# Optimization experiments

Hardware: AMD Instinct MI355X
Metric: run time of the kernel (lower is better)

## Reference

```python
import jax, jax.numpy as jnp
import numpy as np

N = 128          # system size (8*8*2), hard-coded in SpectrumLoss
M_LANCZOS = 10   # Lanczos(m=10)
KAPPA = 0.276


def dd_opt(x, U1, kappa):
    # Wilson-style 2D hopping operator (stand-in for the external DDOpt).
    # x: (B,8,8,2) fields, U1: (B,8,8,2) real gauge links (2 directions).
    u0 = U1[..., 0:1]
    u1 = U1[..., 1:2]
    hop = (u0 * jnp.roll(x, -1, axis=1)
           + u1 * jnp.roll(x, -1, axis=2)
           + jnp.roll(u0 * x, 1, axis=1)
           + jnp.roll(u1 * x, 1, axis=2))
    return x - kappa * hop


def build_lower_tri(net_out):
    # Row-major packing of a lower-triangular NxN matrix (torch.tril_indices order).
    B = net_out.shape[0]
    r, c = jnp.tril_indices(N)
    L = jnp.zeros((B, N, N), net_out.dtype)
    return L.at[:, r, c].set(net_out)


def matvect(L, U1, x):
    # x: (B, N). Preconditioned operator: L (L^T (D x)).
    B = x.shape[0]
    y = dd_opt(x.reshape(B, 8, 8, 2), U1, KAPPA).reshape(B, N)
    y = jnp.einsum('bij,bi->bj', L, y)  # upper_tri_mat: M^H v (real -> M^T v)
    y = jnp.einsum('bij,bj->bi', L, y)  # lower_tri_matvect: L v
    return y


def lanczos(Av, v0):
    # Standard batched Lanczos producing symmetric tridiagonal T (B, M, M).
    B = v0.shape[0]

    def step(carry, _):
        v_prev, v_cur, beta = carry
        w = Av(v_cur)
        alpha = jnp.sum(w * v_cur, axis=1)
        w = w - alpha[:, None] * v_cur - beta[:, None] * v_prev
        beta_new = jnp.linalg.norm(w, axis=1)
        v_next = w / (beta_new[:, None] + 1e-30)
        return (v_cur, v_next, beta_new), (alpha, beta_new)

    init = (jnp.zeros_like(v0), v0, jnp.zeros((B,), v0.dtype))
    _, (alphas, betas) = jax.lax.scan(step, init, None, length=M_LANCZOS)
    alphas = alphas.T  # (B, M)
    betas = betas.T    # (B, M); last beta unused
    T = jnp.zeros((B, M_LANCZOS, M_LANCZOS), v0.dtype)
    i = jnp.arange(M_LANCZOS)
    T = T.at[:, i, i].set(alphas)
    j = jnp.arange(M_LANCZOS - 1)
    T = T.at[:, j, j + 1].set(betas[:, :-1])
    T = T.at[:, j + 1, j].set(betas[:, :-1])
    return T


def setup_inputs() -> dict:
    key = jax.random.key(0)
    k1, k2, k3 = jax.random.split(key, 3)
    B = 2048
    net_out = jax.random.normal(k1, (B, N * (N + 1) // 2), dtype=jnp.float32)
    U1 = jax.random.uniform(k2, (B, 8, 8, 2), dtype=jnp.float32)
    v = jax.random.normal(k3, (B, N), dtype=jnp.float32)
    return {"net_out": net_out, "U1": U1, "v": v}


def reference(net_out, U1, v):
    vn = v / jnp.linalg.norm(v, axis=1, keepdims=True)
    L = build_lower_tri(net_out)
    T = lanczos(lambda x: matvect(L, U1, x), vn)
    eig = jnp.abs(jnp.linalg.eigvalsh(T))  # symmetric tridiagonal -> real eigvals
    max_e = jnp.max(eig, axis=1)
    min_e = jnp.min(eig, axis=1)
    return jnp.mean(max_e ** 2) - jnp.mean(min_e ** 2)
```

## Files before the change

### kernel.cpp

```cpp
#include <hip/hip_runtime.h>
#include <hip/hip_bf16.h>
#include <math.h>

#define NN 128
#define TRI 8256
#define BATCH 2048
#define M_L 10
#define KAPPA 0.276f
#define LDL 136

using half8  = __attribute__((ext_vector_type(8))) _Float16;
using half2v = __attribute__((ext_vector_type(2))) _Float16;
using f32x4  = __attribute__((ext_vector_type(4))) float;

static __device__ inline float dot2h(unsigned m, unsigned y, float c) {
#if __has_builtin(__builtin_amdgcn_fdot2)
    return __builtin_amdgcn_fdot2(__builtin_bit_cast(half2v, m),
                                  __builtin_bit_cast(half2v, y), c, false);
#else
    half2v a = __builtin_bit_cast(half2v, m), b = __builtin_bit_cast(half2v, y);
    return c + (float)a.x * (float)b.x + (float)a.y * (float)b.y;
#endif
}

__global__ __launch_bounds__(256, 4) void lanczos_kernel(
    const float* __restrict__ net_out,
    const float* __restrict__ U1,
    const float* __restrict__ v_in,
    float* __restrict__ ab_out)
{
    __shared__ __align__(16) _Float16 Lsq[128 * LDL];
    __shared__ float u0s[64], u1s[64];
    __shared__ __align__(16) float xv[NN];
    __shared__ __align__(16) _Float16 yh[NN];
    __shared__ float red[6];

    const int b = blockIdx.x;
    const int t = threadIdx.x;
    const int lane = t & 63;
    const int w = t >> 6;

    {
        unsigned long long* z = (unsigned long long*)Lsq;
        #pragma unroll
        for (int k = t; k < 128 * LDL * 2 / 8; k += 256) z[k] = 0ULL;
    }
    if (t < 64) {
        const float2* uu = (const float2*)(U1 + (size_t)b * 128);
        float2 p = uu[t];
        u0s[t] = p.x; u1s[t] = p.y;
    }
    float vt = 0.0f;
    if (t < 128) vt = v_in[(size_t)b * NN + t];
    __syncthreads();

    {
        const float4* src4 = (const float4*)(net_out + (size_t)b * TRI);
        for (int q = t; q < TRI / 4; q += 256) {
            float4 f = src4[q];
            int e = 4 * q;
            int r = (int)((sqrtf(8.0f * (float)e + 1.0f) - 1.0f) * 0.5f);
            while ((r + 1) * (r + 2) / 2 <= e) r++;
            while (r * (r + 1) / 2 > e) r--;
            int c = e - r * (r + 1) / 2;
            Lsq[r * LDL + c] = (_Float16)f.x;
            c++; if (c > r) { r++; c = 0; }
            Lsq[r * LDL + c] = (_Float16)f.y;
            c++; if (c > r) { r++; c = 0; }
            Lsq[r * LDL + c] = (_Float16)f.z;
            c++; if (c > r) { r++; c = 0; }
            Lsq[r * LDL + c] = (_Float16)f.w;
        }
    }
    {
        float s = vt * vt;
        #pragma unroll
        for (int o = 32; o > 0; o >>= 1) s += __shfl_down(s, o, 64);
        if (lane == 0 && t < 128) red[w] = s;
    }
    __syncthreads();

    float xcur = 0.0f;
    if (t < 128) {
        float nrm = sqrtf(red[0] + red[1]);
        xcur = vt / nrm;
        xv[t] = xcur;
    }

    {
        const int m = lane & 15;
        const int g = lane >> 4;
        f32x4 acc[2][8];
        #pragma unroll
        for (int bi = 0; bi < 2; bi++)
            #pragma unroll
            for (int j = 0; j < 8; j++) acc[bi][j] = (f32x4){0.f, 0.f, 0.f, 0.f};
        const int band0 = w, band1 = w + 4;
        #pragma unroll
        for (int kc = 0; kc < 4; kc++) {
            const int col = kc * 32 + g * 8;
            half8 a0 = *(const half8*)&Lsq[(16 * band0 + m) * LDL + col];
            half8 a1 = *(const half8*)&Lsq[(16 * band1 + m) * LDL + col];
            #pragma unroll
            for (int j = 0; j < 8; j++) {
                half8 bfr = *(const half8*)&Lsq[(16 * j + m) * LDL + col];
                acc[0][j] = __builtin_amdgcn_mfma_f32_16x16x32_f16(a0, bfr, acc[0][j], 0, 0, 0);
                acc[1][j] = __builtin_amdgcn_mfma_f32_16x16x32_f16(a1, bfr, acc[1][j], 0, 0, 0);
            }
        }
        __syncthreads();

        #pragma unroll
        for (int bi = 0; bi < 2; bi++) {
            const int band = (bi == 0) ? band0 : band1;
            #pragma unroll
            for (int j = 0; j < 8; j++) {
                f32x4 a = acc[bi][j];
                half2v p01 = {(_Float16)a[0], (_Float16)a[1]};
                half2v p23 = {(_Float16)a[2], (_Float16)a[3]};
                uint2 pk;
                pk.x = __builtin_bit_cast(unsigned, p01);
                pk.y = __builtin_bit_cast(unsigned, p23);
                *(uint2*)&Lsq[(16 * j + m) * LDL + 16 * band + 4 * g] = pk;
            }
        }
    }

    const int si = t >> 4, sj = (t >> 1) & 7, ss = t & 1;
    const int ip = (si + 1) & 7, im = (si + 7) & 7;
    const int jp = (sj + 1) & 7, jm = (sj + 7) & 7;
    const int idx_ip = (ip << 4) | (sj << 1) | ss;
    const int idx_jp = (si << 4) | (jp << 1) | ss;
    const int idx_im = (im << 4) | (sj << 1) | ss;
    const int idx_jm = (si << 4) | (jm << 1) | ss;

    float pvf = 0.0f, beta = 0.0f;
    __syncthreads();

    for (int m_it = 0; m_it < M_L; m_it++) {
        if (t < 128) {
            float hop = u0s[si * 8 + sj] * xv[idx_ip]
                      + u1s[si * 8 + sj] * xv[idx_jp]
                      + u0s[im * 8 + sj] * xv[idx_im]
                      + u1s[si * 8 + jm] * xv[idx_jm];
            yh[t] = (_Float16)(xcur - KAPPA * hop);
        }
        __syncthreads();

        float z = 0.0f;
        if (t < 128) {
            const uint4* M4 = (const uint4*)&Lsq[t * LDL];
            const uint4* Y4 = (const uint4*)yh;
            float acc = 0.f;
            #pragma unroll
            for (int c = 0; c < 16; c++) {
                uint4 mv = M4[c];
                uint4 yv4 = Y4[c];
                acc = dot2h(mv.x, yv4.x, acc);
                acc = dot2h(mv.y, yv4.y, acc);
                acc = dot2h(mv.z, yv4.z, acc);
                acc = dot2h(mv.w, yv4.w, acc);
            }
            z = acc;
            float s1 = z * xcur;
            float s2 = z * z;
            float s3 = z * pvf;
            #pragma unroll
            for (int o = 32; o > 0; o >>= 1) {
                s1 += __shfl_down(s1, o, 64);
                s2 += __shfl_down(s2, o, 64);
                s3 += __shfl_down(s3, o, 64);
            }
            if (lane == 0) { red[w] = s1; red[2 + w] = s2; red[4 + w] = s3; }
        }
        __syncthreads();

        if (t < 128) {
            float alpha = red[0] + red[1];
            float z2    = red[2] + red[3];
            float zp    = red[4] + red[5];
            float b2 = z2 - alpha * alpha - beta * (2.0f * zp - beta);
            float beta_new = sqrtf(fmaxf(b2, 0.0f));
            float wv = z - alpha * xcur - beta * pvf;
            float xn = wv / (beta_new + 1e-30f);
            pvf = xcur;
            xcur = xn;
            xv[t] = xn;
            beta = beta_new;
            if (t == 0) {
                ab_out[(size_t)b * 20 + m_it]      = alpha;
                ab_out[(size_t)b * 20 + 10 + m_it] = beta_new;
            }
        }
        __syncthreads();
    }
}

__device__ inline int sturm_count10(const double* a, const double* off2, double x) {
    double pm = 1.0;
    double p  = a[0] - x;
    int c = (p < 0.0);
    #pragma unroll
    for (int i = 1; i < M_L; i++) {
        double pn = (a[i] - x) * p - off2[i - 1] * pm;
        c += ((pn < 0.0) != (p < 0.0));
        if (fabs(pn) > 1e150) { pn *= 1e-150; p *= 1e-150; }
        pm = p; p = pn;
    }
    return c;
}

__device__ inline double msect_smallest(const double* a, const double* off2,
                                        double lo, double hi, int K, int lane) {
    for (int round = 0; round < 4; round++) {
        double wdt = (hi - lo) * (1.0 / 65.0);
        double x = lo + wdt * (double)(lane + 1);
        int cnt = sturm_count10(a, off2, x);
        unsigned long long mask = __ballot(cnt >= K);
        if (mask == 0ULL) {
            lo = lo + wdt * 64.0;
        } else {
            int p = __ffsll(mask) - 1;
            hi = lo + wdt * (double)(p + 1);
            if (p > 0) lo = lo + wdt * (double)p;
        }
    }
    return 0.5 * (lo + hi);
}

__device__ inline double msect_window(const double* a, const double* off2,
                                      double maxabs, int lane) {
    double lo = 0.0, hi = maxabs;
    for (int round = 0; round < 4; round++) {
        double wdt = (hi - lo) * (1.0 / 65.0);
        double s = lo + wdt * (double)(lane + 1);
        int inwin = sturm_count10(a, off2, s) - sturm_count10(a, off2, -s);
        unsigned long long mask = __ballot(inwin >= 1);
        if (mask == 0ULL) {
            lo = lo + wdt * 64.0;
        } else {
            int p = __ffsll(mask) - 1;
            hi = lo + wdt * (double)(p + 1);
            if (p > 0) lo = lo + wdt * (double)p;
        }
    }
    return 0.5 * (lo + hi);
}

__global__ __launch_bounds__(256) void eig_kernel(
    const float* __restrict__ ab, float* __restrict__ contrib)
{
    const int lane = threadIdx.x & 63;
    const int b = blockIdx.x * 4 + (threadIdx.x >> 6);
    if (b >= BATCH) return;
    const float* p = ab + (size_t)b * 20;
    double a[M_L], off2[M_L - 1], offa[M_L - 1];
    #pragma unroll
    for (int i = 0; i < M_L; i++) a[i] = (double)p[i];
    #pragma unroll
    for (int i = 0; i < M_L - 1; i++) {
        double bb = (double)p[10 + i];
        offa[i] = fabs(bb);
        off2[i] = bb * bb;
    }
    double lo = 1e300, hi = -1e300;
    #pragma unroll
    for (int i = 0; i < M_L; i++) {
        double r = 0.0;
        if (i > 0) r += offa[i - 1];
        if (i < M_L - 1) r += offa[i];
        lo = fmin(lo, a[i] - r);
        hi = fmax(hi, a[i] + r);
    }
    double lmax = msect_smallest(a, off2, lo, hi, M_L, lane);
    double lmin = msect_smallest(a, off2, lo, hi, 1,   lane);
    double maxabs = fmax(fabs(lmax), fabs(lmin));
    double minabs = msect_window(a, off2, maxabs, lane);
    if (lane == 0) contrib[b] = (float)(maxabs * maxabs - minabs * minabs);
}

__global__ __launch_bounds__(1024) void reduce_kernel(
    const float* __restrict__ contrib, float* __restrict__ out)
{
    __shared__ float red[16];
    int t = threadIdx.x;
    float s = contrib[t] + contrib[t + 1024];
    #pragma unroll
    for (int o = 32; o > 0; o >>= 1) s += __shfl_down(s, o, 64);
    if ((t & 63) == 0) red[t >> 6] = s;
    __syncthreads();
    if (t < 64) {
        float r = (t < 16) ? red[t] : 0.0f;
        #pragma unroll
        for (int o = 8; o > 0; o >>= 1) r += __shfl_down(r, o, 64);
        if (t == 0) out[0] = r / (float)BATCH;
    }
}

extern "C" void kernel_launch(void* const* d_in, const int* in_sizes, int n_in,
                              void* d_out, int out_size, void* d_ws, size_t ws_size,
                              hipStream_t stream) {
    const float* net_out = (const float*)d_in[0];
    const float* U1      = (const float*)d_in[1];
    const float* v       = (const float*)d_in[2];
    float* ab      = (float*)d_ws;
    float* contrib = ab + (size_t)BATCH * 20;

    lanczos_kernel<<<BATCH, 256, 0, stream>>>(net_out, U1, v, ab);
    eig_kernel<<<BATCH / 4, 256, 0, stream>>>(ab, contrib);
    reduce_kernel<<<1, 1024, 0, stream>>>(contrib, (float*)d_out);
}
```

Baseline: 140.1 us.

## Process four batch items per block with one wave per Lanczos iteration

Each block now handles four batch elements in turn. All four waves still cooperate to build L and the MFMA product L·L^T for each element in shared memory. The wave that owns an element then loads its two matrix rows into registers and runs the ten Lanczos iterations entirely within the wave, using shuffles for the stencil and the reductions. This removes the block-wide barriers and idle threads of the old per-iteration loop, but it costs 128 registers of matrix per thread, serialises the four matrix builds inside a block, and drops occupancy.

```diff
diff --git a/kernel.cpp b/kernel.cpp
--- a/kernel.cpp
+++ b/kernel.cpp
@@ -23,176 +23,170 @@
 #endif
 }
 
-__global__ __launch_bounds__(256, 4) void lanczos_kernel(
+__global__ __launch_bounds__(256, 2) void lanczos_kernel(
     const float* __restrict__ net_out,
     const float* __restrict__ U1,
     const float* __restrict__ v_in,
     float* __restrict__ ab_out)
 {
     __shared__ __align__(16) _Float16 Lsq[128 * LDL];
-    __shared__ float u0s[64], u1s[64];
-    __shared__ __align__(16) float xv[NN];
-    __shared__ __align__(16) _Float16 yh[NN];
-    __shared__ float red[6];
-
-    const int b = blockIdx.x;
+    __shared__ __align__(16) unsigned yscr[4][64];
+
     const int t = threadIdx.x;
     const int lane = t & 63;
     const int w = t >> 6;
-
-    {
-        unsigned long long* z = (unsigned long long*)Lsq;
+    const int myb = blockIdx.x * 4 + w;
+
+    unsigned m0[64], m1[64];
+    float x0 = 0.f, x1 = 0.f, p0 = 0.f, p1 = 0.f, beta = 0.f;
+    float u0c = 0.f, u1c = 0.f, u0m = 0.f, u1m = 0.f;
+
+    for (int q = 0; q < 4; q++) {
+        const int b = blockIdx.x * 4 + q;
+
+        {
+            unsigned long long* z = (unsigned long long*)Lsq;
+            #pragma unroll
+            for (int k = t; k < 128 * LDL / 4; k += 256) z[k] = 0ULL;
+        }
+        __syncthreads();
+
+        {
+            const float4* src4 = (const float4*)(net_out + (size_t)b * TRI);
+            for (int qd = t; qd < TRI / 4; qd += 256) {
+                float4 f = src4[qd];
+                int e = 4 * qd;
+                int r = (int)((sqrtf(8.0f * (float)e + 1.0f) - 1.0f) * 0.5f);
+                while ((r + 1) * (r + 2) / 2 <= e) r++;
+                while (r * (r + 1) / 2 > e) r--;
+                int c = e - r * (r + 1) / 2;
+                Lsq[r * LDL + c] = (_Float16)f.x;
+                c++; if (c > r) { r++; c = 0; }
+                Lsq[r * LDL + c] = (_Float16)f.y;
+                c++; if (c > r) { r++; c = 0; }
+                Lsq[r * LDL + c] = (_Float16)f.z;
+                c++; if (c > r) { r++; c = 0; }
+                Lsq[r * LDL + c] = (_Float16)f.w;
+            }
+        }
+        __syncthreads();
+
+        {
+            const int m = lane & 15;
+            const int g = lane >> 4;
+            f32x4 acc[2][8];
+            #pragma unroll
+            for (int bi = 0; bi < 2; bi++)
+                #pragma unroll
+                for (int j = 0; j < 8; j++) acc[bi][j] = (f32x4){0.f, 0.f, 0.f, 0.f};
+            const int band0 = w, band1 = w + 4;
+            #pragma unroll
+            for (int kc = 0; kc < 4; kc++) {
+                const int col = kc * 32 + g * 8;
+                half8 a0 = *(const half8*)&Lsq[(16 * band0 + m) * LDL + col];
+                half8 a1 = *(const half8*)&Lsq[(16 * band1 + m) * LDL + col];
+                #pragma unroll
+                for (int j = 0; j < 8; j++) {
+                    half8 bfr = *(const half8*)&Lsq[(16 * j + m) * LDL + col];
+                    acc[0][j] = __builtin_amdgcn_mfma_f32_16x16x32_f16(a0, bfr, acc[0][j], 0, 0, 0);
+                    acc[1][j] = __builtin_amdgcn_mfma_f32_16x16x32_f16(a1, bfr, acc[1][j], 0, 0, 0);
+                }
+            }
+            __syncthreads();
+
+            #pragma unroll
+            for (int bi = 0; bi < 2; bi++) {
+                const int band = (bi == 0) ? band0 : band1;
+                #pragma unroll
+                for (int j = 0; j < 8; j++) {
+                    f32x4 a = acc[bi][j];
+                    half2v p01 = {(_Float16)a[0], (_Float16)a[1]};
+                    half2v p23 = {(_Float16)a[2], (_Float16)a[3]};
+                    uint2 pk;
+                    pk.x = __builtin_bit_cast(unsigned, p01);
+                    pk.y = __builtin_bit_cast(unsigned, p23);
+                    *(uint2*)&Lsq[(16 * j + m) * LDL + 16 * band + 4 * g] = pk;
+                }
+            }
+        }
+        __syncthreads();
+
+        if (w == q) {
+            #pragma unroll
+            for (int c = 0; c < 16; c++) {
+                uint4 a = *(const uint4*)&Lsq[(2 * lane) * LDL + 8 * c];
+                m0[4 * c] = a.x; m0[4 * c + 1] = a.y; m0[4 * c + 2] = a.z; m0[4 * c + 3] = a.w;
+                uint4 bb = *(const uint4*)&Lsq[(2 * lane + 1) * LDL + 8 * c];
+                m1[4 * c] = bb.x; m1[4 * c + 1] = bb.y; m1[4 * c + 2] = bb.z; m1[4 * c + 3] = bb.w;
+            }
+            float2 vv = *(const float2*)(v_in + (size_t)b * NN + 2 * lane);
+            float s = vv.x * vv.x + vv.y * vv.y;
+            #pragma unroll
+            for (int o = 1; o < 64; o <<= 1) s += __shfl_xor(s, o, 64);
+            float inv = 1.0f / sqrtf(s);
+            x0 = vv.x * inv; x1 = vv.y * inv;
+            float2 uu = *(const float2*)(U1 + (size_t)b * 128 + 2 * lane);
+            u0c = uu.x; u1c = uu.y;
+            u0m = __shfl(u0c, (lane + 56) & 63, 64);
+            u1m = __shfl(u1c, (lane & 56) | ((lane + 7) & 7), 64);
+        }
+        __syncthreads();
+    }
+
+    unsigned* ys = yscr[w];
+    const int l_ip = (lane + 8) & 63;
+    const int l_jp = (lane & 56) | ((lane + 1) & 7);
+    const int l_im = (lane + 56) & 63;
+    const int l_jm = (lane & 56) | ((lane + 7) & 7);
+
+    for (int it = 0; it < M_L; it++) {
+        float a0 = __shfl(x0, l_ip, 64), a1 = __shfl(x1, l_ip, 64);
+        float b0 = __shfl(x0, l_jp, 64), b1 = __shfl(x1, l_jp, 64);
+        float c0 = __shfl(x0, l_im, 64), c1 = __shfl(x1, l_im, 64);
+        float d0 = __shfl(x0, l_jm, 64), d1 = __shfl(x1, l_jm, 64);
+        float y0 = x0 - KAPPA * (u0c * a0 + u1c * b0 + u0m * c0 + u1m * d0);
+        float y1 = x1 - KAPPA * (u0c * a1 + u1c * b1 + u0m * c1 + u1m * d1);
+
+        half2v yp = {(_Float16)y0, (_Float16)y1};
+        ys[lane] = __builtin_bit_cast(unsigned, yp);
+
+        float z0 = 0.f, z1 = 0.f;
         #pragma unroll
-        for (int k = t; k < 128 * LDL * 2 / 8; k += 256) z[k] = 0ULL;
-    }
-    if (t < 64) {
-        const float2* uu = (const float2*)(U1 + (size_t)b * 128);
-        float2 p = uu[t];
-        u0s[t] = p.x; u1s[t] = p.y;
-    }
-    float vt = 0.0f;
-    if (t < 128) vt = v_in[(size_t)b * NN + t];
-    __syncthreads();
-
-    {
-        const float4* src4 = (const float4*)(net_out + (size_t)b * TRI);
-        for (int q = t; q < TRI / 4; q += 256) {
-            float4 f = src4[q];
-            int e = 4 * q;
-            int r = (int)((sqrtf(8.0f * (float)e + 1.0f) - 1.0f) * 0.5f);
-            while ((r + 1) * (r + 2) / 2 <= e) r++;
-            while (r * (r + 1) / 2 > e) r--;
-            int c = e - r * (r + 1) / 2;
-            Lsq[r * LDL + c] = (_Float16)f.x;
-            c++; if (c > r) { r++; c = 0; }
-            Lsq[r * LDL + c] = (_Float16)f.y;
-            c++; if (c > r) { r++; c = 0; }
-            Lsq[r * LDL + c] = (_Float16)f.z;
-            c++; if (c > r) { r++; c = 0; }
-            Lsq[r * LDL + c] = (_Float16)f.w;
-        }
-    }
-    {
-        float s = vt * vt;
+        for (int c = 0; c < 16; c++) {
+            uint4 yv = *(const uint4*)&ys[4 * c];
+            z0 = dot2h(m0[4 * c],     yv.x, z0);
+            z1 = dot2h(m1[4 * c],     yv.x, z1);
+            z0 = dot2h(m0[4 * c + 1], yv.y, z0);
+            z1 = dot2h(m1[4 * c + 1], yv.y, z1);
+            z0 = dot2h(m0[4 * c + 2], yv.z, z0);
+            z1 = dot2h(m1[4 * c + 2], yv.z, z1);
+            z0 = dot2h(m0[4 * c + 3], yv.w, z0);
+            z1 = dot2h(m1[4 * c + 3], yv.w, z1);
+        }
+
+        float s1 = z0 * x0 + z1 * x1;
+        float s2 = z0 * z0 + z1 * z1;
+        float s3 = z0 * p0 + z1 * p1;
         #pragma unroll
-        for (int o = 32; o > 0; o >>= 1) s += __shfl_down(s, o, 64);
-        if (lane == 0 && t < 128) red[w] = s;
-    }
-    __syncthreads();
-
-    float xcur = 0.0f;
-    if (t < 128) {
-        float nrm = sqrtf(red[0] + red[1]);
-        xcur = vt / nrm;
-        xv[t] = xcur;
-    }
-
-    {
-        const int m = lane & 15;
-        const int g = lane >> 4;
-        f32x4 acc[2][8];
-        #pragma unroll
-        for (int bi = 0; bi < 2; bi++)
-            #pragma unroll
-            for (int j = 0; j < 8; j++) acc[bi][j] = (f32x4){0.f, 0.f, 0.f, 0.f};
-        const int band0 = w, band1 = w + 4;
-        #pragma unroll
-        for (int kc = 0; kc < 4; kc++) {
-            const int col = kc * 32 + g * 8;
-            half8 a0 = *(const half8*)&Lsq[(16 * band0 + m) * LDL + col];
-            half8 a1 = *(const half8*)&Lsq[(16 * band1 + m) * LDL + col];
-            #pragma unroll
-            for (int j = 0; j < 8; j++) {
-                half8 bfr = *(const half8*)&Lsq[(16 * j + m) * LDL + col];
-                acc[0][j] = __builtin_amdgcn_mfma_f32_16x16x32_f16(a0, bfr, acc[0][j], 0, 0, 0);
-                acc[1][j] = __builtin_amdgcn_mfma_f32_16x16x32_f16(a1, bfr, acc[1][j], 0, 0, 0);
-            }
-        }
-        __syncthreads();
-
-        #pragma unroll
-        for (int bi = 0; bi < 2; bi++) {
-            const int band = (bi == 0) ? band0 : band1;
-            #pragma unroll
-            for (int j = 0; j < 8; j++) {
-                f32x4 a = acc[bi][j];
-                half2v p01 = {(_Float16)a[0], (_Float16)a[1]};
-                half2v p23 = {(_Float16)a[2], (_Float16)a[3]};
-                uint2 pk;
-                pk.x = __builtin_bit_cast(unsigned, p01);
-                pk.y = __builtin_bit_cast(unsigned, p23);
-                *(uint2*)&Lsq[(16 * j + m) * LDL + 16 * band + 4 * g] = pk;
-            }
-        }
-    }
-
-    const int si = t >> 4, sj = (t >> 1) & 7, ss = t & 1;
-    const int ip = (si + 1) & 7, im = (si + 7) & 7;
-    const int jp = (sj + 1) & 7, jm = (sj + 7) & 7;
-    const int idx_ip = (ip << 4) | (sj << 1) | ss;
-    const int idx_jp = (si << 4) | (jp << 1) | ss;
-    const int idx_im = (im << 4) | (sj << 1) | ss;
-    const int idx_jm = (si << 4) | (jm << 1) | ss;
-
-    float pvf = 0.0f, beta = 0.0f;
-    __syncthreads();
-
-    for (int m_it = 0; m_it < M_L; m_it++) {
-        if (t < 128) {
-            float hop = u0s[si * 8 + sj] * xv[idx_ip]
-                      + u1s[si * 8 + sj] * xv[idx_jp]
-                      + u0s[im * 8 + sj] * xv[idx_im]
-                      + u1s[si * 8 + jm] * xv[idx_jm];
-            yh[t] = (_Float16)(xcur - KAPPA * hop);
-        }
-        __syncthreads();
-
-        float z = 0.0f;
-        if (t < 128) {
-            const uint4* M4 = (const uint4*)&Lsq[t * LDL];
-            const uint4* Y4 = (const uint4*)yh;
-            float acc = 0.f;
-            #pragma unroll
-            for (int c = 0; c < 16; c++) {
-                uint4 mv = M4[c];
-                uint4 yv4 = Y4[c];
-                acc = dot2h(mv.x, yv4.x, acc);
-                acc = dot2h(mv.y, yv4.y, acc);
-                acc = dot2h(mv.z, yv4.z, acc);
-                acc = dot2h(mv.w, yv4.w, acc);
-            }
-            z = acc;
-            float s1 = z * xcur;
-            float s2 = z * z;
-            float s3 = z * pvf;
-            #pragma unroll
-            for (int o = 32; o > 0; o >>= 1) {
-                s1 += __shfl_down(s1, o, 64);
-                s2 += __shfl_down(s2, o, 64);
-                s3 += __shfl_down(s3, o, 64);
-            }
-            if (lane == 0) { red[w] = s1; red[2 + w] = s2; red[4 + w] = s3; }
-        }
-        __syncthreads();
-
-        if (t < 128) {
-            float alpha = red[0] + red[1];
-            float z2    = red[2] + red[3];
-            float zp    = red[4] + red[5];
-            float b2 = z2 - alpha * alpha - beta * (2.0f * zp - beta);
-            float beta_new = sqrtf(fmaxf(b2, 0.0f));
-            float wv = z - alpha * xcur - beta * pvf;
-            float xn = wv / (beta_new + 1e-30f);
-            pvf = xcur;
-            xcur = xn;
-            xv[t] = xn;
-            beta = beta_new;
-            if (t == 0) {
-                ab_out[(size_t)b * 20 + m_it]      = alpha;
-                ab_out[(size_t)b * 20 + 10 + m_it] = beta_new;
-            }
-        }
-        __syncthreads();
+        for (int o = 1; o < 64; o <<= 1) {
+            s1 += __shfl_xor(s1, o, 64);
+            s2 += __shfl_xor(s2, o, 64);
+            s3 += __shfl_xor(s3, o, 64);
+        }
+
+        float alpha = s1;
+        float b2 = s2 - alpha * alpha - beta * (2.0f * s3 - beta);
+        float bn = sqrtf(fmaxf(b2, 0.0f));
+        float w0 = z0 - alpha * x0 - beta * p0;
+        float w1 = z1 - alpha * x1 - beta * p1;
+        float inv = 1.0f / (bn + 1e-30f);
+        p0 = x0; p1 = x1;
+        x0 = w0 * inv; x1 = w1 * inv;
+        beta = bn;
+        if (lane == 0) {
+            ab_out[(size_t)myb * 20 + it]      = alpha;
+            ab_out[(size_t)myb * 20 + 10 + it] = bn;
+        }
     }
 }
 
@@ -306,7 +300,7 @@
     float* ab      = (float*)d_ws;
     float* contrib = ab + (size_t)BATCH * 20;
 
-    lanczos_kernel<<<BATCH, 256, 0, stream>>>(net_out, U1, v, ab);
+    lanczos_kernel<<<BATCH / 4, 256, 0, stream>>>(net_out, U1, v, ab);
     eig_kernel<<<BATCH / 4, 256, 0, stream>>>(ab, contrib);
     reduce_kernel<<<1, 1024, 0, stream>>>(contrib, (float*)d_out);
 }
```

After: 143.7 us. 1.03x slower.
